# Kernel tuning notes

Hardware: AMD Instinct MI355X
Metric: run time of the kernel (lower is better)

Reference implementation:

```python
import jax, jax.numpy as jnp
import numpy as np

N = 40000      # nodes
E = 640000     # edges (avg degree 16)
F = 128        # in_feats
OUT = 128      # out_feats


def setup_inputs() -> dict:
    key = jax.random.key(0)
    ks = jax.random.split(key, 8)
    feat = jax.random.normal(ks[0], (N, F), dtype=jnp.float32)
    src = jax.random.randint(ks[1], (E,), 0, N, dtype=jnp.int32)
    dst = jnp.sort(jax.random.randint(ks[2], (E,), 0, N, dtype=jnp.int32))
    # AttentionAGG: fc1 (2F -> F), fc2 (F -> 1); fc_layer (2F -> OUT)
    s1 = 1.0 / np.sqrt(2 * F)
    s2 = 1.0 / np.sqrt(F)
    w1 = jax.random.normal(ks[3], (2 * F, F), dtype=jnp.float32) * s1
    b1 = jnp.zeros((F,), dtype=jnp.float32)
    w2 = jax.random.normal(ks[4], (F, 1), dtype=jnp.float32) * s2
    b2 = jnp.zeros((1,), dtype=jnp.float32)
    wf = jax.random.normal(ks[5], (2 * F, OUT), dtype=jnp.float32) * s1
    bf = jnp.zeros((OUT,), dtype=jnp.float32)
    return {"feat": feat, "src": src, "dst": dst,
            "w1": w1, "b1": b1, "w2": w2, "b2": b2, "wf": wf, "bf": bf}


def reference(feat, src, dst, w1, b1, w2, b2, wf, bf):
    f = feat.shape[1]
    n = feat.shape[0]
    # fc1(concat(h_dst, m_src)) == h_dst @ w1[:F] + h_src @ w1[F:]  (edge_weight is None)
    proj_dst = feat @ w1[:f]          # [N, F]
    proj_src = feat @ w1[f:]          # [N, F]
    pre = jnp.tanh(proj_dst[dst] + proj_src[src] + b1)   # [E, F]
    scores = (pre @ w2)[:, 0] + b2[0]                    # [E]
    # softmax over the ragged incoming-edge set of each dst node
    smax = jax.ops.segment_max(scores, dst, num_segments=n, indices_are_sorted=True)
    ex = jnp.exp(scores - jax.lax.stop_gradient(smax)[dst])
    den = jax.ops.segment_sum(ex, dst, num_segments=n, indices_are_sorted=True)
    att = ex / den[dst]                                  # [E]
    # weighted segment-sum of messages (m_e = feat[src]); zero-degree nodes get 0
    neigh = jax.ops.segment_sum(att[:, None] * feat[src], dst,
                                num_segments=n, indices_are_sorted=True)  # [N, F]
    # fc_layer(concat(h_self, neigh))
    rst = feat @ wf[:f] + neigh @ wf[f:] + bf            # [N, OUT]
    return rst
```

## Files before the change

kernel.cpp:

```cpp
#include <hip/hip_runtime.h>
#include <math.h>

#define F 128
#define OUT 128

typedef unsigned short ushort_t;
typedef __attribute__((ext_vector_type(8))) short bfrag;
typedef __attribute__((ext_vector_type(4))) float ffrag;
typedef __attribute__((ext_vector_type(2))) float fx2;

__device__ __forceinline__ float bf_lo(unsigned int u) {
    return __uint_as_float(u << 16);
}
__device__ __forceinline__ float bf_hi(unsigned int u) {
    return __uint_as_float(u & 0xffff0000u);
}
__device__ __forceinline__ ushort_t f2bf(float f) {
    unsigned int x = __float_as_uint(f);
    unsigned int r = x + 0x7fffu + ((x >> 16) & 1u);
    return (ushort_t)(r >> 16);
}
__device__ __forceinline__ unsigned pk2(float lo, float hi) {
    return (unsigned)f2bf(lo) | ((unsigned)f2bf(hi) << 16);
}

#define DPP_ADD(x, ctrl) \
    ((x) + __int_as_float(__builtin_amdgcn_update_dpp( \
        0, __float_as_int(x), (ctrl), 0xf, 0xf, true)))


__global__ __launch_bounds__(256) void prep_kernel(
    const float* __restrict__ feat, const float* __restrict__ w1,
    const float* __restrict__ wf, const int* __restrict__ dst,
    ushort_t* __restrict__ abig, ushort_t* __restrict__ srcpack,
    ushort_t* __restrict__ btp, ushort_t* __restrict__ btf,
    int* __restrict__ row_ptr, int n, int e, int nb0, int nb1, int nb2)
{
    const int b = blockIdx.x, t = threadIdx.x;
    if (b < nb0) {
        int i = b * 256 + t;
        if (i >= n * 16) return;
        int row = i >> 4, c = (i & 15) * 8;
        float4 a = *(const float4*)(feat + (size_t)row * F + c);
        float4 bb = *(const float4*)(feat + (size_t)row * F + c + 4);
        unsigned p0 = pk2(a.x, a.y), p1 = pk2(a.z, a.w);
        unsigned p2 = pk2(bb.x, bb.y), p3 = pk2(bb.z, bb.w);
        *(uint4*)(abig + (size_t)row * 256 + c) = make_uint4(p0, p1, p2, p3);
        unsigned w01 = (unsigned)__builtin_amdgcn_cvt_pk_fp8_f32(a.x, a.y, 0, false);
        w01 = (unsigned)__builtin_amdgcn_cvt_pk_fp8_f32(a.z, a.w, (int)w01, true);
        unsigned w23 = (unsigned)__builtin_amdgcn_cvt_pk_fp8_f32(bb.x, bb.y, 0, false);
        w23 = (unsigned)__builtin_amdgcn_cvt_pk_fp8_f32(bb.z, bb.w, (int)w23, true);
        char* rb = (char*)srcpack + (size_t)row * 256;
        *(unsigned*)(rb + c * 2 + 4) = w01;
        *(unsigned*)(rb + c * 2 + 12) = w23;
    } else if (b < nb0 + nb1) {
        int idx = (b - nb0) * 256 + t;
        int j = idx >> 7, k = idx & 127;
        float v = (j < F) ? w1[(size_t)k * F + j]
                          : w1[(size_t)(F + k) * F + (j - F)];
        btp[idx] = f2bf(v);
    } else if (b < nb0 + nb1 + nb2) {
        int idx = (b - nb0 - nb1) * 256 + t;
        int j = idx >> 8, k = idx & 255;
        btf[idx] = f2bf(wf[(size_t)k * F + j]);
    } else {
        int i = (b - nb0 - nb1 - nb2) * 256 + t;
        if (i >= e) return;
        int d = dst[i];
        int prev = (i == 0) ? -1 : dst[i - 1];
        for (int v = prev + 1; v <= d; ++v) row_ptr[v] = i;
        if (i == e - 1) {
            for (int v = d + 1; v <= n; ++v) row_ptr[v] = e;
        }
    }
}

#define PST 136
__global__ __launch_bounds__(256) void proj_gemm_kernel(
    const ushort_t* __restrict__ abig, const ushort_t* __restrict__ btp,
    const float* __restrict__ b1, ushort_t* __restrict__ e_dst,
    ushort_t* __restrict__ srcpack, int n)
{
    __shared__ ushort_t As[64 * PST];
    __shared__ ushort_t Ep[4][16 * 80];
    const int t = threadIdx.x;
    const int wv = t >> 6, lane = t & 63;
    const int lm = lane & 15, quad = lane >> 4;
    const int row0 = blockIdx.x * 64, col0 = wv * 64;

#pragma unroll
    for (int k = 0; k < 4; ++k) {
        int l = k * 256 + t;
        int r = l >> 4, ch = l & 15;
        uint4 d = make_uint4(0, 0, 0, 0);
        if (row0 + r < n) d = *(const uint4*)(abig + (size_t)(row0 + r) * 256 + ch * 8);
        *(uint4*)(As + r * PST + ch * 8) = d;
    }
    __syncthreads();

    bfrag bfr[4][4];
#pragma unroll
    for (int ks = 0; ks < 4; ++ks)
#pragma unroll
        for (int ni = 0; ni < 4; ++ni)
            bfr[ks][ni] = *(const bfrag*)(btp + (size_t)(col0 + ni * 16 + lm) * 128
                                          + ks * 32 + quad * 8);

    ffrag acc[4][4];
#pragma unroll
    for (int mi = 0; mi < 4; ++mi)
#pragma unroll
        for (int ni = 0; ni < 4; ++ni) acc[mi][ni] = (ffrag){0.f, 0.f, 0.f, 0.f};

#pragma unroll
    for (int ks = 0; ks < 4; ++ks)
#pragma unroll
        for (int mi = 0; mi < 4; ++mi) {
            bfrag af = *(const bfrag*)(As + (mi * 16 + lm) * PST + ks * 32 + quad * 8);
#pragma unroll
            for (int ni = 0; ni < 4; ++ni)
                acc[mi][ni] = __builtin_amdgcn_mfma_f32_16x16x32_bf16(
                    af, bfr[ks][ni], acc[mi][ni], 0, 0, 0);
        }

    float bias[4];
#pragma unroll
    for (int ni = 0; ni < 4; ++ni)
        bias[ni] = (col0 < F) ? b1[col0 + ni * 16 + lm] : 0.f;

#pragma unroll
    for (int mi = 0; mi < 4; ++mi) {
#pragma unroll
        for (int ni = 0; ni < 4; ++ni)
#pragma unroll
            for (int r = 0; r < 4; ++r)
                Ep[wv][(quad * 4 + r) * 80 + ni * 16 + lm] =
                    f2bf(__expf(2.f * (acc[mi][ni][r] + bias[ni])));
#pragma unroll
        for (int ps = 0; ps < 2; ++ps) {
            int rl = ps * 8 + (lane >> 3), co = (lane & 7) * 8;
            uint4 vv = *(const uint4*)(&Ep[wv][rl * 80 + co]);
            int grow = row0 + mi * 16 + rl;
            if (grow < n) {
                if (col0 < F) {
                    *(uint4*)(e_dst + (size_t)grow * F + col0 + co) = vv;
                } else {
                    int f0 = col0 - F + co;
                    unsigned b0 = (unsigned)__builtin_amdgcn_cvt_pk_bf8_f32(
                        bf_lo(vv.x), bf_hi(vv.x), 0, false);
                    b0 = (unsigned)__builtin_amdgcn_cvt_pk_bf8_f32(
                        bf_lo(vv.y), bf_hi(vv.y), (int)b0, true);
                    unsigned b1v = (unsigned)__builtin_amdgcn_cvt_pk_bf8_f32(
                        bf_lo(vv.z), bf_hi(vv.z), 0, false);
                    b1v = (unsigned)__builtin_amdgcn_cvt_pk_bf8_f32(
                        bf_lo(vv.w), bf_hi(vv.w), (int)b1v, true);
                    char* rb = (char*)srcpack + (size_t)grow * 256;
                    *(unsigned*)(rb + f0 * 2) = b0;
                    *(unsigned*)(rb + f0 * 2 + 8) = b1v;
                }
            }
        }
    }
}

__global__ __launch_bounds__(256) void fused_kernel(
    const ushort_t* __restrict__ e_dst, const ushort_t* __restrict__ srcpack,
    const int* __restrict__ src, const int* __restrict__ row_ptr,
    const float* __restrict__ w2, ushort_t* __restrict__ abig, int n)
{
    const int v = (int)((blockIdx.x * 256u + threadIdx.x) >> 5);
    const int fl = threadIdx.x & 31;
    const int sbase = threadIdx.x & 32;

    const float4 wv4 = ((const float4*)w2)[fl];
    const float w0 = wv4.x, w1_ = wv4.y, w2_ = wv4.z, w3_ = wv4.w;
    float sw = w0 + w1_ + w2_ + w3_;
    float aw = fabsf(w0) + fabsf(w1_) + fabsf(w2_) + fabsf(w3_);
#pragma unroll
    for (int off = 16; off; off >>= 1) {
        sw += __shfl_xor(sw, off, 64);
        aw += __shfl_xor(aw, off, 64);
    }
    const float K = sw - aw;
    const float L2E = 1.4426950408889634f;
    const float K2 = K * L2E;

    if (v >= n) return;
    const int begin = row_ptr[v], end = row_ptr[v + 1];

    const uint2 ud = *(const uint2*)(e_dst + (size_t)v * F + fl * 4);
    const float ea0 = bf_lo(ud.x), ea1 = bf_hi(ud.x);
    const float ea2 = bf_lo(ud.y), ea3 = bf_hi(ud.y);

    const uint2* __restrict__ sp = (const uint2*)srcpack + fl;

    float s = 0.f, a0 = 0.f, a1 = 0.f, a2 = 0.f, a3 = 0.f;

    for (int cb = begin; cb < end; cb += 32) {
        const int clen = min(32, end - cb);
        const int sv = (fl < clen) ? src[cb + fl] : 0;
        int jj = 0;
        for (; jj + 4 <= clen; jj += 4) {
            uint2 u[4];
#pragma unroll
            for (int q = 0; q < 4; ++q) {
                const int sq = __shfl(sv, sbase + jj + q, 64);
                u[q] = sp[(size_t)sq * 32];
            }
            float p[4];
#pragma unroll
            for (int q = 0; q < 4; ++q) {
                fx2 eslo = __builtin_amdgcn_cvt_pk_f32_bf8((int)u[q].x, false);
                fx2 eshi = __builtin_amdgcn_cvt_pk_f32_bf8((int)u[q].x, true);
                float A = fmaf(ea0, eslo[0], 1.f);
                float B = fmaf(ea1, eslo[1], 1.f);
                float C = fmaf(ea2, eshi[0], 1.f);
                float D = fmaf(ea3, eshi[1], 1.f);
                float nAB = fmaf(w0, B, w1_ * A);
                float nCD = fmaf(w2_, D, w3_ * C);
                float rAB = __builtin_amdgcn_rcpf(A * B);
                float rCD = __builtin_amdgcn_rcpf(C * D);
                p[q] = fmaf(nAB, rAB, nCD * rCD);
            }
#pragma unroll
            for (int q = 0; q < 4; ++q) {
                p[q] = DPP_ADD(p[q], 0x121);
                p[q] = DPP_ADD(p[q], 0x122);
                p[q] = DPP_ADD(p[q], 0x124);
                p[q] = DPP_ADD(p[q], 0x128);
                p[q] += __shfl_xor(p[q], 16, 64);
            }
            float g[4];
#pragma unroll
            for (int q = 0; q < 4; ++q)
                g[q] = exp2f(fmaf(-2.f * L2E, p[q], K2));
            s += (g[0] + g[1]) + (g[2] + g[3]);
#pragma unroll
            for (int q = 0; q < 4; ++q) {
                fx2 lo = __builtin_amdgcn_cvt_pk_f32_fp8((int)u[q].y, false);
                fx2 hi = __builtin_amdgcn_cvt_pk_f32_fp8((int)u[q].y, true);
                a0 = fmaf(g[q], lo[0], a0);
                a1 = fmaf(g[q], lo[1], a1);
                a2 = fmaf(g[q], hi[0], a2);
                a3 = fmaf(g[q], hi[1], a3);
            }
        }
        for (; jj < clen; ++jj) {
            const int s0 = __shfl(sv, sbase + jj, 64);
            const uint2 u0 = sp[(size_t)s0 * 32];
            fx2 eslo = __builtin_amdgcn_cvt_pk_f32_bf8((int)u0.x, false);
            fx2 eshi = __builtin_amdgcn_cvt_pk_f32_bf8((int)u0.x, true);
            float A = fmaf(ea0, eslo[0], 1.f);
            float B = fmaf(ea1, eslo[1], 1.f);
            float C = fmaf(ea2, eshi[0], 1.f);
            float D = fmaf(ea3, eshi[1], 1.f);
            float nAB = fmaf(w0, B, w1_ * A);
            float nCD = fmaf(w2_, D, w3_ * C);
            float rAB = __builtin_amdgcn_rcpf(A * B);
            float rCD = __builtin_amdgcn_rcpf(C * D);
            float p0 = fmaf(nAB, rAB, nCD * rCD);
            p0 = DPP_ADD(p0, 0x121);
            p0 = DPP_ADD(p0, 0x122);
            p0 = DPP_ADD(p0, 0x124);
            p0 = DPP_ADD(p0, 0x128);
            p0 += __shfl_xor(p0, 16, 64);
            const float g0 = exp2f(fmaf(-2.f * L2E, p0, K2));
            s += g0;
            fx2 lo = __builtin_amdgcn_cvt_pk_f32_fp8((int)u0.y, false);
            fx2 hi = __builtin_amdgcn_cvt_pk_f32_fp8((int)u0.y, true);
            a0 = fmaf(g0, lo[0], a0);
            a1 = fmaf(g0, lo[1], a1);
            a2 = fmaf(g0, hi[0], a2);
            a3 = fmaf(g0, hi[1], a3);
        }
    }

    const float inv = (end > begin) ? 1.f / s : 0.f;
    ushort4 o = make_ushort4(f2bf(a0 * inv), f2bf(a1 * inv),
                             f2bf(a2 * inv), f2bf(a3 * inv));
    *(ushort4*)(abig + (size_t)v * 256 + 128 + fl * 4) = o;
}

#define OST 280
__global__ __launch_bounds__(256) void out_gemm_kernel(
    const ushort_t* __restrict__ abig, const ushort_t* __restrict__ btf,
    const float* __restrict__ bfv, float* __restrict__ out, int n)
{
    __shared__ ushort_t As[64 * OST];
    const int t = threadIdx.x;
    const int wv = t >> 6, lane = t & 63;
    const int lm = lane & 15, quad = lane >> 4;
    const int row0 = blockIdx.x * 64, col0 = wv * 32;

#pragma unroll
    for (int k = 0; k < 8; ++k) {
        int l = k * 256 + t;
        int r = l >> 5, ch = l & 31;
        uint4 d = make_uint4(0, 0, 0, 0);
        if (row0 + r < n) d = *(const uint4*)(abig + (size_t)(row0 + r) * 256 + ch * 8);
        *(uint4*)(As + r * OST + ch * 8) = d;
    }
    __syncthreads();

    bfrag bfr[8][2];
#pragma unroll
    for (int ks = 0; ks < 8; ++ks)
#pragma unroll
        for (int ni = 0; ni < 2; ++ni)
            bfr[ks][ni] = *(const bfrag*)(btf + (size_t)(col0 + ni * 16 + lm) * 256
                                          + ks * 32 + quad * 8);

    ffrag acc[4][2];
#pragma unroll
    for (int mi = 0; mi < 4; ++mi)
#pragma unroll
        for (int ni = 0; ni < 2; ++ni) acc[mi][ni] = (ffrag){0.f, 0.f, 0.f, 0.f};

#pragma unroll
    for (int ks = 0; ks < 8; ++ks)
#pragma unroll
        for (int mi = 0; mi < 4; ++mi) {
            bfrag af = *(const bfrag*)(As + (mi * 16 + lm) * OST + ks * 32 + quad * 8);
#pragma unroll
            for (int ni = 0; ni < 2; ++ni)
                acc[mi][ni] = __builtin_amdgcn_mfma_f32_16x16x32_bf16(
                    af, bfr[ks][ni], acc[mi][ni], 0, 0, 0);
        }

#pragma unroll
    for (int ni = 0; ni < 2; ++ni) {
        const int j = col0 + ni * 16 + lm;
        const float bb = bfv[j];
#pragma unroll
        for (int mi = 0; mi < 4; ++mi)
#pragma unroll
            for (int r = 0; r < 4; ++r) {
                int grow = row0 + mi * 16 + quad * 4 + r;
                if (grow < n) out[(size_t)grow * OUT + j] = acc[mi][ni][r] + bb;
            }
    }
}

extern "C" void kernel_launch(void* const* d_in, const int* in_sizes, int n_in,
                              void* d_out, int out_size, void* d_ws, size_t ws_size,
                              hipStream_t stream)
{
    const float* feat = (const float*)d_in[0];
    const int*   src  = (const int*)d_in[1];
    const int*   dst  = (const int*)d_in[2];
    const float* w1   = (const float*)d_in[3];
    const float* b1   = (const float*)d_in[4];
    const float* w2   = (const float*)d_in[5];
    const float* b2   = (const float*)d_in[6];  (void)b2;
    const float* wf   = (const float*)d_in[7];
    const float* bfv  = (const float*)d_in[8];
    float* out = (float*)d_out;

    const int n = in_sizes[0] / F;
    const int e = in_sizes[1];

    ushort_t* abig    = (ushort_t*)d_ws;
    ushort_t* e_dst   = abig + (size_t)n * 256;
    ushort_t* srcpack = e_dst + (size_t)n * 128;
    ushort_t* btp     = srcpack + (size_t)n * 128;
    ushort_t* btf     = btp + 32768;
    int* row_ptr      = (int*)(btf + 32768);

    const int nb0 = (n * 16 + 255) / 256;
    const int nb1 = 128, nb2 = 128;
    const int nb3 = (e + 255) / 256;

    prep_kernel<<<nb0 + nb1 + nb2 + nb3, 256, 0, stream>>>(
        feat, w1, wf, dst, abig, srcpack, btp, btf, row_ptr, n, e, nb0, nb1, nb2);
    proj_gemm_kernel<<<(n + 63) / 64, 256, 0, stream>>>(
        abig, btp, b1, e_dst, srcpack, n);
    fused_kernel<<<(n + 7) / 8, 256, 0, stream>>>(
        e_dst, srcpack, src, row_ptr, w2, abig, n);
    out_gemm_kernel<<<(n + 63) / 64, 256, 0, stream>>>(abig, btf, bfv, out, n);
}
```

Before: 155.1 us.

## Fuse feature conversion into projection GEMM and stage output stores through LDS

Moves the fp32-to-bf16/fp8 conversion of node features out of the prep kernel and into the projection GEMM's tile load. The GEMM now reads feat directly, which removes the separate write-then-reread of the bf16 copy before the GEMM. The output GEMM epilogue now goes through a per-wave LDS buffer so each lane writes float4 row-contiguous chunks instead of scattered scalar stores. This costs extra LDS space and some shuffling work in the epilogue.

After: 149.9 us. -3.4%, faster.

```diff
diff --git a/kernel.cpp b/kernel.cpp
--- a/kernel.cpp
+++ b/kernel.cpp
@@ -29,42 +29,25 @@
         0, __float_as_int(x), (ctrl), 0xf, 0xf, true)))
 
 
-__global__ __launch_bounds__(256) void prep_kernel(
-    const float* __restrict__ feat, const float* __restrict__ w1,
-    const float* __restrict__ wf, const int* __restrict__ dst,
-    ushort_t* __restrict__ abig, ushort_t* __restrict__ srcpack,
-    ushort_t* __restrict__ btp, ushort_t* __restrict__ btf,
-    int* __restrict__ row_ptr, int n, int e, int nb0, int nb1, int nb2)
+__global__ __launch_bounds__(256) void tiny_prep_kernel(
+    const float* __restrict__ w1, const float* __restrict__ wf,
+    const int* __restrict__ dst, ushort_t* __restrict__ btp,
+    ushort_t* __restrict__ btf, int* __restrict__ row_ptr,
+    int n, int e, int nb1, int nb2)
 {
     const int b = blockIdx.x, t = threadIdx.x;
-    if (b < nb0) {
-        int i = b * 256 + t;
-        if (i >= n * 16) return;
-        int row = i >> 4, c = (i & 15) * 8;
-        float4 a = *(const float4*)(feat + (size_t)row * F + c);
-        float4 bb = *(const float4*)(feat + (size_t)row * F + c + 4);
-        unsigned p0 = pk2(a.x, a.y), p1 = pk2(a.z, a.w);
-        unsigned p2 = pk2(bb.x, bb.y), p3 = pk2(bb.z, bb.w);
-        *(uint4*)(abig + (size_t)row * 256 + c) = make_uint4(p0, p1, p2, p3);
-        unsigned w01 = (unsigned)__builtin_amdgcn_cvt_pk_fp8_f32(a.x, a.y, 0, false);
-        w01 = (unsigned)__builtin_amdgcn_cvt_pk_fp8_f32(a.z, a.w, (int)w01, true);
-        unsigned w23 = (unsigned)__builtin_amdgcn_cvt_pk_fp8_f32(bb.x, bb.y, 0, false);
-        w23 = (unsigned)__builtin_amdgcn_cvt_pk_fp8_f32(bb.z, bb.w, (int)w23, true);
-        char* rb = (char*)srcpack + (size_t)row * 256;
-        *(unsigned*)(rb + c * 2 + 4) = w01;
-        *(unsigned*)(rb + c * 2 + 12) = w23;
-    } else if (b < nb0 + nb1) {
-        int idx = (b - nb0) * 256 + t;
+    if (b < nb1) {
+        int idx = b * 256 + t;
         int j = idx >> 7, k = idx & 127;
         float v = (j < F) ? w1[(size_t)k * F + j]
                           : w1[(size_t)(F + k) * F + (j - F)];
         btp[idx] = f2bf(v);
-    } else if (b < nb0 + nb1 + nb2) {
-        int idx = (b - nb0 - nb1) * 256 + t;
+    } else if (b < nb1 + nb2) {
+        int idx = (b - nb1) * 256 + t;
         int j = idx >> 8, k = idx & 255;
         btf[idx] = f2bf(wf[(size_t)k * F + j]);
     } else {
-        int i = (b - nb0 - nb1 - nb2) * 256 + t;
+        int i = (b - nb1 - nb2) * 256 + t;
         if (i >= e) return;
         int d = dst[i];
         int prev = (i == 0) ? -1 : dst[i - 1];
@@ -77,9 +60,9 @@
 
 #define PST 136
 __global__ __launch_bounds__(256) void proj_gemm_kernel(
-    const ushort_t* __restrict__ abig, const ushort_t* __restrict__ btp,
-    const float* __restrict__ b1, ushort_t* __restrict__ e_dst,
-    ushort_t* __restrict__ srcpack, int n)
+    const float* __restrict__ feat, const ushort_t* __restrict__ btp,
+    const float* __restrict__ b1, ushort_t* __restrict__ abig,
+    ushort_t* __restrict__ e_dst, ushort_t* __restrict__ srcpack, int n)
 {
     __shared__ ushort_t As[64 * PST];
     __shared__ ushort_t Ep[4][16 * 80];
@@ -91,10 +74,27 @@
 #pragma unroll
     for (int k = 0; k < 4; ++k) {
         int l = k * 256 + t;
-        int r = l >> 4, ch = l & 15;
-        uint4 d = make_uint4(0, 0, 0, 0);
-        if (row0 + r < n) d = *(const uint4*)(abig + (size_t)(row0 + r) * 256 + ch * 8);
-        *(uint4*)(As + r * PST + ch * 8) = d;
+        int r = l >> 4, c = (l & 15) * 8;
+        int grow = row0 + r;
+        float4 a = make_float4(0.f, 0.f, 0.f, 0.f);
+        float4 bb = make_float4(0.f, 0.f, 0.f, 0.f);
+        if (grow < n) {
+            a = *(const float4*)(feat + (size_t)grow * F + c);
+            bb = *(const float4*)(feat + (size_t)grow * F + c + 4);
+        }
+        unsigned p0 = pk2(a.x, a.y), p1 = pk2(a.z, a.w);
+        unsigned p2 = pk2(bb.x, bb.y), p3 = pk2(bb.z, bb.w);
+        *(uint4*)(As + r * PST + c) = make_uint4(p0, p1, p2, p3);
+        if (grow < n) {
+            *(uint4*)(abig + (size_t)grow * 256 + c) = make_uint4(p0, p1, p2, p3);
+            unsigned w01 = (unsigned)__builtin_amdgcn_cvt_pk_fp8_f32(a.x, a.y, 0, false);
+            w01 = (unsigned)__builtin_amdgcn_cvt_pk_fp8_f32(a.z, a.w, (int)w01, true);
+            unsigned w23 = (unsigned)__builtin_amdgcn_cvt_pk_fp8_f32(bb.x, bb.y, 0, false);
+            w23 = (unsigned)__builtin_amdgcn_cvt_pk_fp8_f32(bb.z, bb.w, (int)w23, true);
+            char* rb = (char*)srcpack + (size_t)grow * 256;
+            *(unsigned*)(rb + c * 2 + 4) = w01;
+            *(unsigned*)(rb + c * 2 + 12) = w23;
+        }
     }
     __syncthreads();
 
@@ -282,11 +282,13 @@
 }
 
 #define OST 280
+#define EFS 36
 __global__ __launch_bounds__(256) void out_gemm_kernel(
     const ushort_t* __restrict__ abig, const ushort_t* __restrict__ btf,
     const float* __restrict__ bfv, float* __restrict__ out, int n)
 {
     __shared__ ushort_t As[64 * OST];
+    __shared__ float Ef[4][16 * EFS];
     const int t = threadIdx.x;
     const int wv = t >> 6, lane = t & 63;
     const int lm = lane & 15, quad = lane >> 4;
@@ -327,17 +329,25 @@
                     af, bfr[ks][ni], acc[mi][ni], 0, 0, 0);
         }
 
-#pragma unroll
-    for (int ni = 0; ni < 2; ++ni) {
-        const int j = col0 + ni * 16 + lm;
-        const float bb = bfv[j];
-#pragma unroll
-        for (int mi = 0; mi < 4; ++mi)
-#pragma unroll
-            for (int r = 0; r < 4; ++r) {
-                int grow = row0 + mi * 16 + quad * 4 + r;
-                if (grow < n) out[(size_t)grow * OUT + j] = acc[mi][ni][r] + bb;
-            }
+    float bb[2];
+#pragma unroll
+    for (int ni = 0; ni < 2; ++ni) bb[ni] = bfv[col0 + ni * 16 + lm];
+
+#pragma unroll
+    for (int mi = 0; mi < 4; ++mi) {
+#pragma unroll
+        for (int ni = 0; ni < 2; ++ni)
+#pragma unroll
+            for (int r = 0; r < 4; ++r)
+                Ef[wv][(quad * 4 + r) * EFS + ni * 16 + lm] = acc[mi][ni][r] + bb[ni];
+#pragma unroll
+        for (int ps = 0; ps < 2; ++ps) {
+            int rl = ps * 8 + (lane >> 3), co = (lane & 7) * 4;
+            float4 vv = *(const float4*)(&Ef[wv][rl * EFS + co]);
+            int grow = row0 + mi * 16 + rl;
+            if (grow < n)
+                *(float4*)(out + (size_t)grow * OUT + col0 + co) = vv;
+        }
     }
 }
 
@@ -366,14 +376,13 @@
     ushort_t* btf     = btp + 32768;
     int* row_ptr      = (int*)(btf + 32768);
 
-    const int nb0 = (n * 16 + 255) / 256;
     const int nb1 = 128, nb2 = 128;
     const int nb3 = (e + 255) / 256;
 
-    prep_kernel<<<nb0 + nb1 + nb2 + nb3, 256, 0, stream>>>(
-        feat, w1, wf, dst, abig, srcpack, btp, btf, row_ptr, n, e, nb0, nb1, nb2);
+    tiny_prep_kernel<<<nb1 + nb2 + nb3, 256, 0, stream>>>(
+        w1, wf, dst, btp, btf, row_ptr, n, e, nb1, nb2);
     proj_gemm_kernel<<<(n + 63) / 64, 256, 0, stream>>>(
-        abig, btp, b1, e_dst, srcpack, n);
+        feat, btp, b1, abig, e_dst, srcpack, n);
     fused_kernel<<<(n + 7) / 8, 256, 0, stream>>>(
         e_dst, srcpack, src, row_ptr, w2, abig, n);
     out_gemm_kernel<<<(n + 63) / 64, 256, 0, stream>>>(abig, btf, bfv, out, n);
```
